# Kernel optimization log

Measured on AMD Instinct MI355X. Metric: run time of the kernel, lower is better.

Reference implementation:

```python
import jax, jax.numpy as jnp
import numpy as np
from jax import lax

B, C, L, K = 8, 256, 4096, 65
PAD = K // 2  # torch: int(kernel.shape[-1] / 2) = 32 -> same-length output for odd K


def depthwise_corr(x, k):
    """Depthwise cross-correlation (torch conv1d semantics, no kernel flip).
    x: [B, C, L] float32, k: [K] float32 (same kernel shared by all channels,
    matching kernel.repeat(seq_len, 1)). Returns [B, C, L]."""
    w = jnp.broadcast_to(k.reshape(1, 1, K), (C, 1, K))  # [C, 1, K]
    return lax.conv_general_dilated(
        x, w, window_strides=(1,), padding=[(PAD, PAD)],
        dimension_numbers=("NCH", "OIH", "NCH"), feature_group_count=C)


def setup_inputs() -> dict:
    key = jax.random.key(0)
    k1, k2, k3 = jax.random.split(key, 3)
    return {
        "x": jax.random.normal(k1, (B, C, L), dtype=jnp.float32),
        "kernel_real": jax.random.normal(k2, (K,), dtype=jnp.float32),
        "kernel_imag": jax.random.normal(k3, (K,), dtype=jnp.float32),
        "weights_mag": jnp.ones((1, C, 1), dtype=jnp.float32),
        "weights_angle": jnp.ones((1, C, 1), dtype=jnp.float32),
    }


def reference(x, kernel_real, kernel_imag, weights_mag, weights_angle):
    # mf_coeffs = conj(kernel) -> weight = kernel_real - 1j*kernel_imag.
    # Input x is real (imag=0 after .to(complex64)), so complex conv splits
    # into two real depthwise correlations.
    yr = depthwise_corr(x, kernel_real)            # [B, C, L]
    yi = -depthwise_corr(x, kernel_imag)           # [B, C, L]
    y = lax.complex(yr, yi)                        # complex64 [B, C, L]

    # torch.std over dims (1,2), unbiased (correction=1), complex -> real std
    mean = jnp.mean(y, axis=(1, 2), keepdims=True)
    n = C * L
    var = jnp.sum(jnp.abs(y - mean) ** 2, axis=(1, 2), keepdims=True) / (n - 1)
    y = y / jnp.sqrt(var)                          # real std broadcasts over complex

    # weights_mag * y * exp(-1j * weights_angle)
    phase = lax.complex(jnp.cos(weights_angle), -jnp.sin(weights_angle))  # [1, C, 1]
    y = weights_mag * y * phase

    # FFT over the channel dim (dim=-2), then fftshift on that dim
    return jnp.fft.fftshift(jnp.fft.fft(y, axis=-2), axes=-2)
```

## Files before the change

kernel.cpp:

```cpp
#include <hip/hip_runtime.h>
#include <math.h>

#define NB 8
#define NC 256
#define NL 4096
#define NK 65

__device__ float g_stats[NB * 4];

__global__ void zero_stats_kernel() {
    if (threadIdx.x < NB * 4) g_stats[threadIdx.x] = 0.0f;
}

__global__ void finalize_stats_kernel()
{
    int b = threadIdx.x;
    if (b < NB) {
        float sr = g_stats[b*4+0], si = g_stats[b*4+1], sq = g_stats[b*4+2];
        const float n = (float)(NC * NL);
        float var = (sq - (sr*sr + si*si)/n) / (n - 1.0f);
        g_stats[b*4+3] = rsqrtf(var);
    }
}

__global__ __launch_bounds__(256) void fused_conv_fft_kernel(
    const float* __restrict__ x,
    const float* __restrict__ kre,
    const float* __restrict__ kim,
    const float* __restrict__ wmag,
    const float* __restrict__ wang,
    float* __restrict__ out,
    int out_size)
{
    __shared__ __align__(16) float4 lbuf4[NC * 9];
    __shared__ float twr[NC], twi[NC];
    __shared__ float red[12];

    const int t = threadIdx.x;
    const int b = blockIdx.x & 7;
    const int l0 = (blockIdx.x >> 3) << 4;

    {
        float ang = (float)t * 0.024543692606170260f;
        float s, c;
        sincosf(ang, &s, &c);
        twr[t] = c; twi[t] = -s;
    }
    float sw, cw;
    sincosf(wang[t], &sw, &cw);
    const float wm = wmag[t];
    const float wgr =  wm * cw;
    const float wgi = -wm * sw;

    const float* xb = x + (size_t)b * NC * NL;
    const bool interleaved = (out_size >= 2 * NB * NC * NL);

    float sr[16], si[16];
    #pragma unroll
    for (int i = 0; i < 16; ++i) { sr[i] = 0.0f; si[i] = 0.0f; }

    #pragma unroll
    for (int cb = 0; cb < 4; ++cb) {
        __syncthreads();
        #pragma unroll
        for (int it = 0; it < 8; ++it) {
            int fidx = it * 256 + t;
            int rr = fidx >> 3, q = fidx & 7;
            int g0 = l0 + 16 * cb - 32 + 4 * q;
            const float* xr = xb + (size_t)rr * NL;
            float4 v;
            if (g0 >= 0 && g0 <= NL - 4) {
                v = *(const float4*)(xr + g0);
            } else {
                v.x = (g0 + 0 >= 0 && g0 + 0 < NL) ? xr[g0 + 0] : 0.0f;
                v.y = (g0 + 1 >= 0 && g0 + 1 < NL) ? xr[g0 + 1] : 0.0f;
                v.z = (g0 + 2 >= 0 && g0 + 2 < NL) ? xr[g0 + 2] : 0.0f;
                v.w = (g0 + 3 >= 0 && g0 + 3 < NL) ? xr[g0 + 3] : 0.0f;
            }
            lbuf4[rr * 9 + q] = v;
        }
        __syncthreads();
        float w[32];
        #pragma unroll
        for (int q = 0; q < 8; ++q) {
            float4 v = lbuf4[t * 9 + q];
            w[4*q+0] = v.x; w[4*q+1] = v.y; w[4*q+2] = v.z; w[4*q+3] = v.w;
        }
        #pragma unroll
        for (int j2 = 0; j2 < 16; ++j2) {
            const float kr = kre[16 * cb + j2];
            const float ki = kim[16 * cb + j2];
            #pragma unroll
            for (int i = 0; i < 16; ++i) {
                sr[i] = fmaf(w[i + j2], kr, sr[i]);
                si[i] = fmaf(w[i + j2], ki, si[i]);
            }
        }
    }
    __syncthreads();
    #pragma unroll
    for (int it = 0; it < 4; ++it) {
        int fidx = it * 256 + t;
        int rr = fidx >> 2, q = fidx & 3;
        int g0 = l0 + 32 + 4 * q;
        const float* xr = xb + (size_t)rr * NL;
        float4 v;
        if (g0 <= NL - 4) {
            v = *(const float4*)(xr + g0);
        } else {
            v.x = (g0 + 0 < NL) ? xr[g0 + 0] : 0.0f;
            v.y = (g0 + 1 < NL) ? xr[g0 + 1] : 0.0f;
            v.z = (g0 + 2 < NL) ? xr[g0 + 2] : 0.0f;
            v.w = (g0 + 3 < NL) ? xr[g0 + 3] : 0.0f;
        }
        lbuf4[rr * 9 + q] = v;
    }
    __syncthreads();
    {
        float w[16];
        #pragma unroll
        for (int q = 0; q < 4; ++q) {
            float4 v = lbuf4[t * 9 + q];
            w[4*q+0] = v.x; w[4*q+1] = v.y; w[4*q+2] = v.z; w[4*q+3] = v.w;
        }
        const float kr = kre[64];
        const float ki = kim[64];
        #pragma unroll
        for (int i = 0; i < 16; ++i) {
            sr[i] = fmaf(w[i], kr, sr[i]);
            si[i] = fmaf(w[i], ki, si[i]);
        }
    }

    float tsr = 0.0f, tsi = 0.0f, tsq = 0.0f;
    #pragma unroll
    for (int i = 0; i < 16; ++i) {
        tsr += sr[i];
        tsi -= si[i];
        tsq = fmaf(sr[i], sr[i], tsq);
        tsq = fmaf(si[i], si[i], tsq);
    }

    #pragma unroll
    for (int k = 0; k < 8; ++k) {
        float4 o;
        o.x = sr[2*k]   * wgr + si[2*k]   * wgi;
        o.y = sr[2*k]   * wgi - si[2*k]   * wgr;
        o.z = sr[2*k+1] * wgr + si[2*k+1] * wgi;
        o.w = sr[2*k+1] * wgi - si[2*k+1] * wgr;
        lbuf4[t * 9 + k] = o;
    }
    __syncthreads();

    #pragma unroll
    for (int s = 0; s < 4; ++s) {
        const int shift = 2 * s;
        const int q = 64 >> shift;
        #pragma unroll
        for (int it = 0; it < 2; ++it) {
            int task = it * 256 + t;
            int lpp = task & 7;
            int m = task >> 3;
            int j = m & (q - 1);
            int blk = m >> (6 - shift);
            int base2 = blk << (8 - shift);
            int e = j << shift;

            int ca = base2 + j;
            float4 a0 = lbuf4[ca*9 + lpp];
            float4 a1 = lbuf4[(ca + q)*9 + lpp];
            float4 a2 = lbuf4[(ca + 2*q)*9 + lpp];
            float4 a3 = lbuf4[(ca + 3*q)*9 + lpp];

            float w1r = twr[e],   w1i = twi[e];
            float w2r = twr[2*e], w2i = twi[2*e];
            float w3r = twr[3*e], w3i = twi[3*e];

            float4 b0, b1, b2, b3;
            {
                float t0r = a0.x + a2.x, t0i = a0.y + a2.y;
                float t1r = a0.x - a2.x, t1i = a0.y - a2.y;
                float t2r = a1.x + a3.x, t2i = a1.y + a3.y;
                float t3r = a1.x - a3.x, t3i = a1.y - a3.y;
                b0.x = t0r + t2r;       b0.y = t0i + t2i;
                float b2r = t0r - t2r,  b2i = t0i - t2i;
                float b1r = t1r + t3i,  b1i = t1i - t3r;
                float b3r = t1r - t3i,  b3i = t1i + t3r;
                b1.x = b1r*w1r - b1i*w1i;  b1.y = b1r*w1i + b1i*w1r;
                b2.x = b2r*w2r - b2i*w2i;  b2.y = b2r*w2i + b2i*w2r;
                b3.x = b3r*w3r - b3i*w3i;  b3.y = b3r*w3i + b3i*w3r;
            }
            {
                float t0r = a0.z + a2.z, t0i = a0.w + a2.w;
                float t1r = a0.z - a2.z, t1i = a0.w - a2.w;
                float t2r = a1.z + a3.z, t2i = a1.w + a3.w;
                float t3r = a1.z - a3.z, t3i = a1.w - a3.w;
                b0.z = t0r + t2r;       b0.w = t0i + t2i;
                float b2r = t0r - t2r,  b2i = t0i - t2i;
                float b1r = t1r + t3i,  b1i = t1i - t3r;
                float b3r = t1r - t3i,  b3i = t1i + t3r;
                b1.z = b1r*w1r - b1i*w1i;  b1.w = b1r*w1i + b1i*w1r;
                b2.z = b2r*w2r - b2i*w2i;  b2.w = b2r*w2i + b2i*w2r;
                b3.z = b3r*w3r - b3i*w3i;  b3.w = b3r*w3i + b3i*w3r;
            }
            lbuf4[ca*9 + lpp]         = b0;
            lbuf4[(ca + q)*9 + lpp]   = b1;
            lbuf4[(ca + 2*q)*9 + lpp] = b2;
            lbuf4[(ca + 3*q)*9 + lpp] = b3;
        }
        __syncthreads();
    }

    #pragma unroll
    for (int it = 0; it < 8; ++it) {
        int task = it * 256 + t;
        int lpp = task & 7;
        int pp = task >> 3;
        float4 v = lbuf4[pp*9 + lpp];
        int k = ((pp & 3) << 6) | (((pp >> 2) & 3) << 4)
              | (((pp >> 4) & 3) << 2) | ((pp >> 6) & 3);
        int cout = k ^ 128;
        if (interleaved) {
            size_t fi = 2 * ((size_t)(b * NC + cout) * NL + l0) + 4 * lpp;
            if (fi + 4 <= (size_t)out_size) *(float4*)(out + fi) = v;
        } else {
            size_t fi = (size_t)(b * NC + cout) * NL + l0 + 2 * lpp;
            if (fi + 2 <= (size_t)out_size) {
                float2 o2; o2.x = v.x; o2.y = v.z;
                *(float2*)(out + fi) = o2;
            }
        }
    }

    #pragma unroll
    for (int off = 32; off > 0; off >>= 1) {
        tsr += __shfl_down(tsr, off);
        tsi += __shfl_down(tsi, off);
        tsq += __shfl_down(tsq, off);
    }
    const int lane = t & 63, wv = t >> 6;
    if (lane == 0) { red[wv*3+0] = tsr; red[wv*3+1] = tsi; red[wv*3+2] = tsq; }
    __syncthreads();
    if (t == 0) {
        float a0 = 0.0f, a1 = 0.0f, a2 = 0.0f;
        for (int i = 0; i < 4; ++i) { a0 += red[i*3]; a1 += red[i*3+1]; a2 += red[i*3+2]; }
        atomicAdd(&g_stats[b*4+0], a0);
        atomicAdd(&g_stats[b*4+1], a1);
        atomicAdd(&g_stats[b*4+2], a2);
    }
}

__global__ __launch_bounds__(256) void scale_out_kernel(
    float* __restrict__ out, int out_size)
{
    const int chunk = out_size >> 3;
    const int n4 = out_size >> 2;
    float4* o4 = (float4*)out;
    for (int i4 = blockIdx.x * blockDim.x + threadIdx.x; i4 < n4;
         i4 += gridDim.x * blockDim.x) {
        int b = (i4 << 2) / chunk;
        float inv = g_stats[b*4+3];
        float4 v = o4[i4];
        v.x *= inv; v.y *= inv; v.z *= inv; v.w *= inv;
        o4[i4] = v;
    }
    int tail0 = n4 << 2;
    int ti = tail0 + blockIdx.x * blockDim.x + threadIdx.x;
    if (ti < out_size) {
        int b = ti / chunk;
        out[ti] *= g_stats[b*4+3];
    }
}

extern "C" void kernel_launch(void* const* d_in, const int* in_sizes, int n_in,
                              void* d_out, int out_size, void* d_ws, size_t ws_size,
                              hipStream_t stream)
{
    const float* x   = (const float*)d_in[0];
    const float* kre = (const float*)d_in[1];
    const float* kim = (const float*)d_in[2];
    const float* wm  = (const float*)d_in[3];
    const float* wa  = (const float*)d_in[4];
    float* out = (float*)d_out;
    (void)d_ws; (void)ws_size;

    zero_stats_kernel<<<1, 64, 0, stream>>>();
    fused_conv_fft_kernel<<<NB * (NL / 16), 256, 0, stream>>>(x, kre, kim, wm, wa,
                                                              out, out_size);
    finalize_stats_kernel<<<1, 64, 0, stream>>>();
    scale_out_kernel<<<2048, 256, 0, stream>>>(out, out_size);
}
```

Measured before the change: 162.3 us.

## Load conv window directly from global into registers; fold stats finalize into scale kernel

The conv stage no longer stages input tiles through shared memory with block-wide barriers. Each thread now loads its own channel's window straight from global memory into two rotating 16-float register buffers, interleaving loads with the FMA chunks. Separately, the finalize-stats kernel is removed: each block of the scale kernel computes the per-batch inverse std into shared memory, and a shift replaces the integer divide when the chunk size is a power of two. The trade is that each thread now reads a strided per-channel row, so global loads across threads are uncoalesced and lean on cache hits. It does remove one kernel launch and all barriers from the conv loop.

```diff
diff --git a/kernel.cpp b/kernel.cpp
--- a/kernel.cpp
+++ b/kernel.cpp
@@ -12,16 +12,41 @@
     if (threadIdx.x < NB * 4) g_stats[threadIdx.x] = 0.0f;
 }
 
-__global__ void finalize_stats_kernel()
-{
-    int b = threadIdx.x;
-    if (b < NB) {
-        float sr = g_stats[b*4+0], si = g_stats[b*4+1], sq = g_stats[b*4+2];
-        const float n = (float)(NC * NL);
-        float var = (sq - (sr*sr + si*si)/n) / (n - 1.0f);
-        g_stats[b*4+3] = rsqrtf(var);
-    }
-}
+
+#define LOAD16(W, off)                                                      \
+    {                                                                       \
+        const int g0_ = l0 + (off);                                         \
+        if (g0_ >= 0 && g0_ + 16 <= NL) {         \
+            _Pragma("unroll")                                               \
+            for (int q = 0; q < 4; ++q) {                                   \
+                const float4 v_ = *(const float4*)(xr + g0_ + 4 * q);       \
+                W[4*q+0] = v_.x; W[4*q+1] = v_.y;                           \
+                W[4*q+2] = v_.z; W[4*q+3] = v_.w;                           \
+            }                                                               \
+        } else {                                                            \
+            _Pragma("unroll")                                               \
+            for (int q = 0; q < 16; ++q) {                                  \
+                const int g_ = g0_ + q;                                     \
+                W[q] = (g_ >= 0 && g_ < NL) ? xr[g_] : 0.0f;                \
+            }                                                               \
+        }                                                                   \
+    }
+
+#define CHUNK16(Lo, Hi, tb)                                                 \
+    {                                                                       \
+        _Pragma("unroll")                                                   \
+        for (int j2 = 0; j2 < 16; ++j2) {                                   \
+            const float kr_ = kre[(tb) + j2];        \
+            const float ki_ = kim[(tb) + j2];                               \
+            _Pragma("unroll")                                               \
+            for (int i = 0; i < 16; ++i) {                                  \
+                const int wi_ = i + j2;                                     \
+                const float xv_ = (wi_ < 16) ? Lo[wi_] : Hi[wi_ - 16];      \
+                sr[i] = fmaf(xv_, kr_, sr[i]);                              \
+                si[i] = fmaf(xv_, ki_, si[i]);                              \
+            }                                                               \
+        }                                                                   \
+    }
 
 __global__ __launch_bounds__(256) void fused_conv_fft_kernel(
     const float* __restrict__ x,
@@ -52,83 +77,30 @@
     const float wgr =  wm * cw;
     const float wgi = -wm * sw;
 
-    const float* xb = x + (size_t)b * NC * NL;
+    const float* xr = x + (size_t)b * NC * NL + (size_t)t * NL;
     const bool interleaved = (out_size >= 2 * NB * NC * NL);
 
     float sr[16], si[16];
     #pragma unroll
     for (int i = 0; i < 16; ++i) { sr[i] = 0.0f; si[i] = 0.0f; }
 
-    #pragma unroll
-    for (int cb = 0; cb < 4; ++cb) {
-        __syncthreads();
-        #pragma unroll
-        for (int it = 0; it < 8; ++it) {
-            int fidx = it * 256 + t;
-            int rr = fidx >> 3, q = fidx & 7;
-            int g0 = l0 + 16 * cb - 32 + 4 * q;
-            const float* xr = xb + (size_t)rr * NL;
-            float4 v;
-            if (g0 >= 0 && g0 <= NL - 4) {
-                v = *(const float4*)(xr + g0);
-            } else {
-                v.x = (g0 + 0 >= 0 && g0 + 0 < NL) ? xr[g0 + 0] : 0.0f;
-                v.y = (g0 + 1 >= 0 && g0 + 1 < NL) ? xr[g0 + 1] : 0.0f;
-                v.z = (g0 + 2 >= 0 && g0 + 2 < NL) ? xr[g0 + 2] : 0.0f;
-                v.w = (g0 + 3 >= 0 && g0 + 3 < NL) ? xr[g0 + 3] : 0.0f;
-            }
-            lbuf4[rr * 9 + q] = v;
-        }
-        __syncthreads();
-        float w[32];
-        #pragma unroll
-        for (int q = 0; q < 8; ++q) {
-            float4 v = lbuf4[t * 9 + q];
-            w[4*q+0] = v.x; w[4*q+1] = v.y; w[4*q+2] = v.z; w[4*q+3] = v.w;
-        }
-        #pragma unroll
-        for (int j2 = 0; j2 < 16; ++j2) {
-            const float kr = kre[16 * cb + j2];
-            const float ki = kim[16 * cb + j2];
-            #pragma unroll
-            for (int i = 0; i < 16; ++i) {
-                sr[i] = fmaf(w[i + j2], kr, sr[i]);
-                si[i] = fmaf(w[i + j2], ki, si[i]);
-            }
-        }
-    }
-    __syncthreads();
-    #pragma unroll
-    for (int it = 0; it < 4; ++it) {
-        int fidx = it * 256 + t;
-        int rr = fidx >> 2, q = fidx & 3;
-        int g0 = l0 + 32 + 4 * q;
-        const float* xr = xb + (size_t)rr * NL;
-        float4 v;
-        if (g0 <= NL - 4) {
-            v = *(const float4*)(xr + g0);
-        } else {
-            v.x = (g0 + 0 < NL) ? xr[g0 + 0] : 0.0f;
-            v.y = (g0 + 1 < NL) ? xr[g0 + 1] : 0.0f;
-            v.z = (g0 + 2 < NL) ? xr[g0 + 2] : 0.0f;
-            v.w = (g0 + 3 < NL) ? xr[g0 + 3] : 0.0f;
-        }
-        lbuf4[rr * 9 + q] = v;
-    }
-    __syncthreads();
+    float A[16], B[16];
+    LOAD16(A, -32);
+    LOAD16(B, -16);
+    CHUNK16(A, B, 0);
+    LOAD16(A, 0);
+    CHUNK16(B, A, 16);
+    LOAD16(B, 16);
+    CHUNK16(A, B, 32);
+    LOAD16(A, 32);
+    CHUNK16(B, A, 48);
     {
-        float w[16];
-        #pragma unroll
-        for (int q = 0; q < 4; ++q) {
-            float4 v = lbuf4[t * 9 + q];
-            w[4*q+0] = v.x; w[4*q+1] = v.y; w[4*q+2] = v.z; w[4*q+3] = v.w;
-        }
-        const float kr = kre[64];
-        const float ki = kim[64];
+        const float kr_ = kre[64];
+        const float ki_ = kim[64];
         #pragma unroll
         for (int i = 0; i < 16; ++i) {
-            sr[i] = fmaf(w[i], kr, sr[i]);
-            si[i] = fmaf(w[i], ki, si[i]);
+            sr[i] = fmaf(A[i], kr_, sr[i]);
+            si[i] = fmaf(A[i], ki_, si[i]);
         }
     }
 
@@ -253,22 +225,35 @@
 __global__ __launch_bounds__(256) void scale_out_kernel(
     float* __restrict__ out, int out_size)
 {
+    __shared__ float sinv[NB];
+    const int t = threadIdx.x;
+    if (t < NB) {
+        float sr = g_stats[t*4+0], si = g_stats[t*4+1], sq = g_stats[t*4+2];
+        const float n = (float)(NC * NL);
+        float var = (sq - (sr*sr + si*si)/n) / (n - 1.0f);
+        sinv[t] = rsqrtf(var);
+    }
+    __syncthreads();
+
     const int chunk = out_size >> 3;
+    const bool p2 = (chunk & (chunk - 1)) == 0;
+    const int lb = 31 - __clz(chunk);
     const int n4 = out_size >> 2;
     float4* o4 = (float4*)out;
-    for (int i4 = blockIdx.x * blockDim.x + threadIdx.x; i4 < n4;
+    for (int i4 = blockIdx.x * blockDim.x + t; i4 < n4;
          i4 += gridDim.x * blockDim.x) {
-        int b = (i4 << 2) / chunk;
-        float inv = g_stats[b*4+3];
+        int fi = i4 << 2;
+        int bidx = p2 ? (fi >> lb) : (fi / chunk);
+        float inv = sinv[bidx];
         float4 v = o4[i4];
         v.x *= inv; v.y *= inv; v.z *= inv; v.w *= inv;
         o4[i4] = v;
     }
     int tail0 = n4 << 2;
-    int ti = tail0 + blockIdx.x * blockDim.x + threadIdx.x;
+    int ti = tail0 + blockIdx.x * blockDim.x + t;
     if (ti < out_size) {
-        int b = ti / chunk;
-        out[ti] *= g_stats[b*4+3];
+        int bidx = p2 ? (ti >> lb) : (ti / chunk);
+        out[ti] *= sinv[bidx];
     }
 }
 
@@ -287,6 +272,5 @@
     zero_stats_kernel<<<1, 64, 0, stream>>>();
     fused_conv_fft_kernel<<<NB * (NL / 16), 256, 0, stream>>>(x, kre, kim, wm, wa,
                                                               out, out_size);
-    finalize_stats_kernel<<<1, 64, 0, stream>>>();
     scale_out_kernel<<<2048, 256, 0, stream>>>(out, out_size);
 }
```

Measured after the change: 151.6 us. 1.07x faster.
